# Performance work log

Measured on AMD Instinct MI355X. Metric: run time of the kernel, lower is better.

Reference implementation:

```python
import jax, jax.numpy as jnp
import numpy as np

N_NODES = 50000
N_EDGES = 800000
NODE_IN, EDGE_IN, HIDDEN, OUT = 64, 16, 128, 32


def _gcn_conv(x, edge_index, W, b, num_nodes):
    """PyG GCNConv: symmetric-normalized aggregation with self-loops.
       out = D^{-1/2} (A + I) D^{-1/2} (x @ W) + b
    """
    h = x @ W                                   # [N, H]
    loop = jnp.arange(num_nodes, dtype=edge_index.dtype)
    row = jnp.concatenate([edge_index[0], loop])  # src
    col = jnp.concatenate([edge_index[1], loop])  # dst
    deg = jax.ops.segment_sum(jnp.ones(row.shape[0], dtype=h.dtype), col,
                              num_segments=num_nodes)
    dinv = jnp.where(deg > 0, jax.lax.rsqrt(deg), 0.0)
    norm = dinv[row] * dinv[col]                # [E+N]
    msg = h[row] * norm[:, None]                # gather + scale
    out = jax.ops.segment_sum(msg, col, num_segments=num_nodes)  # scatter-add
    return out + b


def setup_inputs() -> dict:
    key = jax.random.key(0)
    ks = jax.random.split(key, 8)
    s1 = 1.0 / np.sqrt(NODE_IN)
    s2 = 1.0 / np.sqrt(HIDDEN)
    s3 = 1.0 / np.sqrt(HIDDEN * 2 + EDGE_IN)
    return {
        "x": jax.random.normal(ks[0], (N_NODES, NODE_IN), dtype=jnp.float32),
        "edge_index": jax.random.randint(ks[1], (2, N_EDGES), 0, N_NODES,
                                         dtype=jnp.int64),
        "edge_attr": jax.random.normal(ks[2], (N_EDGES, EDGE_IN),
                                       dtype=jnp.float32),
        "W1": jax.random.normal(ks[3], (NODE_IN, HIDDEN), dtype=jnp.float32) * s1,
        "b1": jnp.zeros((HIDDEN,), dtype=jnp.float32),
        "W2": jax.random.normal(ks[4], (HIDDEN, HIDDEN), dtype=jnp.float32) * s2,
        "b2": jnp.zeros((HIDDEN,), dtype=jnp.float32),
        "W_edge": jax.random.normal(ks[5], (HIDDEN * 2 + EDGE_IN, OUT),
                                    dtype=jnp.float32) * s3,
        "b_edge": jnp.zeros((OUT,), dtype=jnp.float32),
    }


def reference(x, edge_index, edge_attr, W1, b1, W2, b2, W_edge, b_edge):
    n = x.shape[0]
    h = jax.nn.relu(_gcn_conv(x, edge_index, W1, b1, n))
    h = jax.nn.relu(_gcn_conv(h, edge_index, W2, b2, n))
    src, dst = edge_index[0], edge_index[1]
    edge_features = jnp.concatenate([h[src], h[dst], edge_attr], axis=1)
    return edge_features @ W_edge + b_edge
```

## Files before the change

### kernel.cpp

```cpp
#include <hip/hip_runtime.h>

#define NN 50000
#define NE 800000

typedef __attribute__((ext_vector_type(8))) short short8v;
typedef __attribute__((ext_vector_type(4))) float f32x4;

__device__ __forceinline__ float bf_lo(unsigned u) { return __uint_as_float(u << 16); }
__device__ __forceinline__ float bf_hi(unsigned u) { return __uint_as_float(u & 0xffff0000u); }
__device__ __forceinline__ unsigned pack_bf2(float a, float b) {
  unsigned ua = __float_as_uint(a);
  ua = (ua + 0x7fffu + ((ua >> 16) & 1u)) >> 16;
  unsigned ub = __float_as_uint(b);
  ub = (ub + 0x7fffu + ((ub >> 16) & 1u)) & 0xffff0000u;
  return ua | ub;
}
__device__ __forceinline__ unsigned short bf16r(float f) {
  unsigned u = __float_as_uint(f);
  u = (u + 0x7fffu + ((u >> 16) & 1u)) >> 16;
  return (unsigned short)u;
}

__global__ void k_prep0(const float* __restrict__ W1, const float* __restrict__ W2,
                        const float* __restrict__ We,
                        unsigned short* __restrict__ W1t,
                        unsigned short* __restrict__ W2t,
                        unsigned short* __restrict__ Wabt,
                        int* cnt, int* cur) {
  int i = blockIdx.x * 256 + threadIdx.x;
  if (i < NN) { cnt[i] = 0; cur[i] = 0; }
  if (i < 8192)  { int c = i >> 6, k = i & 63;  W1t[i] = bf16r(W1[k * 128 + c]); }
  if (i < 16384) { int c = i >> 7, k = i & 127; W2t[i] = bf16r(W2[k * 128 + c]); }
  if (i < 8192) {
    int c = i >> 7, k = i & 127;
    float v = (c < 32) ? We[k * 32 + c] : We[(128 + k) * 32 + (c - 32)];
    Wabt[i] = bf16r(v);
  }
}

__global__ void k_count(const int* dst, int* cnt, int e) {
  int i = blockIdx.x * blockDim.x + threadIdx.x;
  if (i < e) atomicAdd(&cnt[dst[i]], 1);
}

__global__ void k_scan1(const int* cnt, int* offs, int* bsum, int n) {
  __shared__ int s[256];
  int i = blockIdx.x * 256 + threadIdx.x;
  int v = (i < n) ? cnt[i] : 0;
  s[threadIdx.x] = v;
  __syncthreads();
  #pragma unroll
  for (int d = 1; d < 256; d <<= 1) {
    int t = (threadIdx.x >= d) ? s[threadIdx.x - d] : 0;
    __syncthreads();
    s[threadIdx.x] += t;
    __syncthreads();
  }
  if (i < n) offs[i] = s[threadIdx.x] - v;
  if (threadIdx.x == 255) bsum[blockIdx.x] = s[255];
}

__global__ void k_scan2(int* bsum, int* offsN, int nb) {
  __shared__ int s[256];
  int v = (threadIdx.x < nb) ? bsum[threadIdx.x] : 0;
  s[threadIdx.x] = v;
  __syncthreads();
  #pragma unroll
  for (int d = 1; d < 256; d <<= 1) {
    int t = (threadIdx.x >= d) ? s[threadIdx.x - d] : 0;
    __syncthreads();
    s[threadIdx.x] += t;
    __syncthreads();
  }
  if (threadIdx.x < nb) bsum[threadIdx.x] = s[threadIdx.x] - v;
  if (threadIdx.x == 255) *offsN = s[255];
}

__global__ void k_scan3_dinv(int* offs, const int* bsum, const int* cnt,
                             float* dinv, int n) {
  int i = blockIdx.x * blockDim.x + threadIdx.x;
  if (i < n) {
    offs[i] += bsum[i >> 8];
    dinv[i] = rsqrtf((float)(cnt[i] + 1));
  }
}

__global__ void k_fill(const int* src, const int* dst, const int* offs,
                       int* cur, int* adj, int e) {
  int i = blockIdx.x * blockDim.x + threadIdx.x;
  if (i < e) {
    int d = dst[i];
    int pos = atomicAdd(&cur[d], 1);
    adj[offs[d] + pos] = src[i];
  }
}

__global__ void k_prescale(const float* __restrict__ x,
                           const float* __restrict__ dinv,
                           unsigned* __restrict__ xs, int n) {
  int i = blockIdx.x * blockDim.x + threadIdx.x;
  if (i >= n * 32) return;
  int v = i >> 5, c2 = i & 31;
  float d = dinv[v];
  float2 xv = ((const float2*)(x + (size_t)v * 64))[c2];
  xs[(size_t)v * 32 + c2] = pack_bf2(xv.x * d, xv.y * d);
}

__global__ void k_agg64(const unsigned* __restrict__ xs,
                        const int* __restrict__ offs, const int* __restrict__ adj,
                        const float* __restrict__ dinv, unsigned* __restrict__ z,
                        int n) {
  int node = blockIdx.x * 8 + (threadIdx.x >> 5);
  if (node >= n) return;
  int lane = threadIdx.x & 31;
  float ax[8], ay[8];
  {
    unsigned u = xs[(size_t)node * 32 + lane];
    ax[0] = bf_lo(u); ay[0] = bf_hi(u);
  }
  #pragma unroll
  for (int u = 1; u < 8; u++) { ax[u] = 0.f; ay[u] = 0.f; }
  int s = offs[node], e = offs[node + 1];
  int i = s;
  for (; i + 8 <= e; i += 8) {
    int idx[8];
    #pragma unroll
    for (int u = 0; u < 8; u++) idx[u] = adj[i + u];
    #pragma unroll
    for (int u = 0; u < 8; u++) {
      unsigned uv = xs[(size_t)idx[u] * 32 + lane];
      ax[u] += bf_lo(uv); ay[u] += bf_hi(uv);
    }
  }
  for (; i < e; i++) {
    unsigned uv = xs[(size_t)adj[i] * 32 + lane];
    ax[0] += bf_lo(uv); ay[0] += bf_hi(uv);
  }
  float sx = ((ax[0] + ax[1]) + (ax[2] + ax[3])) + ((ax[4] + ax[5]) + (ax[6] + ax[7]));
  float sy = ((ay[0] + ay[1]) + (ay[2] + ay[3])) + ((ay[4] + ay[5]) + (ay[6] + ay[7]));
  float d = dinv[node];
  z[(size_t)node * 32 + lane] = pack_bf2(sx * d, sy * d);
}

__global__ void k_agg128(const unsigned* __restrict__ hs,
                         const int* __restrict__ offs, const int* __restrict__ adj,
                         const float* __restrict__ dinv, unsigned* __restrict__ z,
                         int n) {
  int node = blockIdx.x * 4 + (threadIdx.x >> 6);
  if (node >= n) return;
  int lane = threadIdx.x & 63;
  float ax[8], ay[8];
  {
    unsigned u = hs[(size_t)node * 64 + lane];
    ax[0] = bf_lo(u); ay[0] = bf_hi(u);
  }
  #pragma unroll
  for (int u = 1; u < 8; u++) { ax[u] = 0.f; ay[u] = 0.f; }
  int s = offs[node], e = offs[node + 1];
  int i = s;
  for (; i + 8 <= e; i += 8) {
    int idx[8];
    #pragma unroll
    for (int u = 0; u < 8; u++) idx[u] = adj[i + u];
    #pragma unroll
    for (int u = 0; u < 8; u++) {
      unsigned uv = hs[(size_t)idx[u] * 64 + lane];
      ax[u] += bf_lo(uv); ay[u] += bf_hi(uv);
    }
  }
  for (; i < e; i++) {
    unsigned uv = hs[(size_t)adj[i] * 64 + lane];
    ax[0] += bf_lo(uv); ay[0] += bf_hi(uv);
  }
  float sx = ((ax[0] + ax[1]) + (ax[2] + ax[3])) + ((ax[4] + ax[5]) + (ax[6] + ax[7]));
  float sy = ((ay[0] + ay[1]) + (ay[2] + ay[3])) + ((ay[4] + ay[5]) + (ay[6] + ay[7]));
  float d = dinv[node];
  z[(size_t)node * 64 + lane] = pack_bf2(sx * d, sy * d);
}

template <int K>
__global__ __launch_bounds__(256) void k_mgemm(const unsigned short* __restrict__ A,
                                               const unsigned short* __restrict__ Bt,
                                               const float* __restrict__ bias,
                                               const float* __restrict__ dinv,
                                               unsigned short* __restrict__ outb,
                                               int n) {
  int lane = threadIdx.x & 63;
  int wid = threadIdx.x >> 6;
  int wr = wid >> 1, wc = wid & 1;
  int r0 = blockIdx.x * 32 + wr * 16;
  int cbase = wc * 64;
  int lr = lane & 15;
  int lk = (lane >> 4) * 8;
  int arow = r0 + lr;
  if (arow >= n) arow = n - 1;
  const unsigned short* arp = A + (size_t)arow * K + lk;
  f32x4 acc[4];
  #pragma unroll
  for (int ct = 0; ct < 4; ct++) acc[ct] = (f32x4){0.f, 0.f, 0.f, 0.f};
  #pragma unroll
  for (int ks = 0; ks < K; ks += 32) {
    short8v a = *reinterpret_cast<const short8v*>(arp + ks);
    #pragma unroll
    for (int ct = 0; ct < 4; ct++) {
      const unsigned short* bp = Bt + (size_t)(cbase + ct * 16 + lr) * K + lk + ks;
      short8v b = *reinterpret_cast<const short8v*>(bp);
      acc[ct] = __builtin_amdgcn_mfma_f32_16x16x32_bf16(a, b, acc[ct], 0, 0, 0);
    }
  }
  int rbase = r0 + (lane >> 4) * 4;
  #pragma unroll
  for (int ct = 0; ct < 4; ct++) {
    int col = cbase + ct * 16 + lr;
    float bv = bias[col];
    #pragma unroll
    for (int rg = 0; rg < 4; rg++) {
      int row = rbase + rg;
      if (row >= n) continue;
      float v = fmaxf(acc[ct][rg] + bv, 0.f);
      outb[(size_t)row * 128 + col] = bf16r(v * dinv[row]);
    }
  }
}

__global__ __launch_bounds__(256) void k_mgemm2pq(
    const unsigned short* __restrict__ A,
    const unsigned short* __restrict__ Bt,
    const unsigned short* __restrict__ Wabt,
    const float* __restrict__ bias,
    unsigned short* __restrict__ PQb,
    int n) {
  __shared__ unsigned short hs[32][136];
  int lane = threadIdx.x & 63;
  int wid = threadIdx.x >> 6;
  int wr = wid >> 1, wc = wid & 1;
  int r0 = blockIdx.x * 32;
  int lr = lane & 15;
  int lk = (lane >> 4) * 8;
  int arow = r0 + wr * 16 + lr;
  if (arow >= n) arow = n - 1;
  const unsigned short* arp = A + (size_t)arow * 128 + lk;
  f32x4 acc[4];
  #pragma unroll
  for (int ct = 0; ct < 4; ct++) acc[ct] = (f32x4){0.f, 0.f, 0.f, 0.f};
  #pragma unroll
  for (int ks = 0; ks < 128; ks += 32) {
    short8v a = *reinterpret_cast<const short8v*>(arp + ks);
    #pragma unroll
    for (int ct = 0; ct < 4; ct++) {
      const unsigned short* bp = Bt + (size_t)(wc * 64 + ct * 16 + lr) * 128 + lk + ks;
      short8v b = *reinterpret_cast<const short8v*>(bp);
      acc[ct] = __builtin_amdgcn_mfma_f32_16x16x32_bf16(a, b, acc[ct], 0, 0, 0);
    }
  }
  int rloc = wr * 16 + (lane >> 4) * 4;
  #pragma unroll
  for (int ct = 0; ct < 4; ct++) {
    int col = wc * 64 + ct * 16 + lr;
    float bv = bias[col];
    #pragma unroll
    for (int rg = 0; rg < 4; rg++)
      hs[rloc + rg][col] = bf16r(fmaxf(acc[ct][rg] + bv, 0.f));
  }
  __syncthreads();
  f32x4 acc2[2];
  acc2[0] = (f32x4){0.f, 0.f, 0.f, 0.f};
  acc2[1] = (f32x4){0.f, 0.f, 0.f, 0.f};
  #pragma unroll
  for (int ks = 0; ks < 128; ks += 32) {
    short8v a2 = *reinterpret_cast<const short8v*>(&hs[wr * 16 + lr][lk + ks]);
    #pragma unroll
    for (int ct = 0; ct < 2; ct++) {
      const unsigned short* wp = Wabt + (size_t)(wc * 32 + ct * 16 + lr) * 128 + lk + ks;
      short8v b = *reinterpret_cast<const short8v*>(wp);
      acc2[ct] = __builtin_amdgcn_mfma_f32_16x16x32_bf16(a2, b, acc2[ct], 0, 0, 0);
    }
  }
  #pragma unroll
  for (int ct = 0; ct < 2; ct++) {
    int col = wc * 32 + ct * 16 + lr;
    #pragma unroll
    for (int rg = 0; rg < 4; rg++) {
      int row = r0 + wr * 16 + (lane >> 4) * 4 + rg;
      if (row < n) PQb[(size_t)row * 64 + col] = bf16r(acc2[ct][rg]);
    }
  }
}

__global__ __launch_bounds__(256) void k_edge5(const int* __restrict__ src,
                                               const int* __restrict__ dst,
                                               const float* __restrict__ ea,
                                               const unsigned* __restrict__ PQw,
                                               const float* __restrict__ We,
                                               const float* __restrict__ be,
                                               float* __restrict__ out, int ne) {
  __shared__ int sidx[64];
  __shared__ int didx[64];
  __shared__ float eas[64][16];
  __shared__ float wcs[16][32];
  __shared__ float bes[32];
  int tid = threadIdx.x;
  int ebase = blockIdx.x * 64;
  if (tid < 128)
    ((float4*)wcs)[tid] = ((const float4*)(We + 256 * 32))[tid];
  if (tid < 32) bes[tid] = be[tid];
  if (tid >= 128 && tid < 192) sidx[tid - 128] = src[ebase + tid - 128];
  if (tid >= 192)              didx[tid - 192] = dst[ebase + tid - 192];
  {
    int row = tid >> 2, q = tid & 3;
    ((float4*)eas[row])[q] = ((const float4*)(ea + (size_t)(ebase + row) * 16))[q];
  }
  __syncthreads();
  int l = tid & 15;
  int grp = tid >> 4;
  unsigned pw[4], qw[4];
  int el[4];
  #pragma unroll
  for (int u = 0; u < 4; u++) el[u] = u * 16 + grp;
  #pragma unroll
  for (int u = 0; u < 4; u++) {
    int s = sidx[el[u]];
    int d = didx[el[u]];
    pw[u] = PQw[(size_t)s * 32 + l];
    qw[u] = PQw[(size_t)d * 32 + 16 + l];
  }
  int c0 = 2 * l;
  #pragma unroll
  for (int u = 0; u < 4; u++) {
    int e = ebase + el[u];
    float a0 = bf_lo(pw[u]) + bf_lo(qw[u]) + bes[c0];
    float a1 = bf_hi(pw[u]) + bf_hi(qw[u]) + bes[c0 + 1];
    #pragma unroll
    for (int k = 0; k < 16; k++) {
      float ev = eas[el[u]][k];
      a0 += ev * wcs[k][c0];
      a1 += ev * wcs[k][c0 + 1];
    }
    ((float2*)(out + (size_t)e * 32))[l] = make_float2(a0, a1);
  }
}

extern "C" void kernel_launch(void* const* d_in, const int* in_sizes, int n_in,
                              void* d_out, int out_size, void* d_ws, size_t ws_size,
                              hipStream_t stream) {
  const float* x  = (const float*)d_in[0];
  const int*   ei = (const int*)d_in[1];
  const float* ea = (const float*)d_in[2];
  const float* W1 = (const float*)d_in[3];
  const float* b1 = (const float*)d_in[4];
  const float* W2 = (const float*)d_in[5];
  const float* b2 = (const float*)d_in[6];
  const float* We = (const float*)d_in[7];
  const float* be = (const float*)d_in[8];
  float* out = (float*)d_out;
  const int* src = ei;
  const int* dst = ei + NE;

  char* w = (char*)d_ws;
  auto alloc = [&](size_t b) {
    void* p = (void*)w;
    w += (b + 255) & ~(size_t)255;
    return p;
  };
  int* cnt    = (int*)alloc(NN * 4);
  int* cur    = (int*)alloc(NN * 4);
  int* offs   = (int*)alloc((NN + 1) * 4);
  int* bsum   = (int*)alloc(256 * 4);
  int* adj    = (int*)alloc((size_t)NE * 4);
  float* dinv = (float*)alloc(NN * 4);
  unsigned* xs  = (unsigned*)alloc((size_t)NN * 32 * 4);
  unsigned* h1s = (unsigned*)alloc((size_t)NN * 64 * 4);
  unsigned* z12 = (unsigned*)alloc((size_t)NN * 64 * 4);
  unsigned short* w1t  = (unsigned short*)alloc(8192 * 2);
  unsigned short* w2t  = (unsigned short*)alloc(16384 * 2);
  unsigned short* wabt = (unsigned short*)alloc(8192 * 2);
  unsigned short* pqb = (unsigned short*)h1s;

  const int nblkN = (NN + 255) / 256;
  const int nblkE = (NE + 255) / 256;

  k_prep0<<<nblkN, 256, 0, stream>>>(W1, W2, We, w1t, w2t, wabt, cnt, cur);
  k_count<<<nblkE, 256, 0, stream>>>(dst, cnt, NE);
  k_scan1<<<nblkN, 256, 0, stream>>>(cnt, offs, bsum, NN);
  k_scan2<<<1, 256, 0, stream>>>(bsum, offs + NN, nblkN);
  k_scan3_dinv<<<nblkN, 256, 0, stream>>>(offs, bsum, cnt, dinv, NN);
  k_fill<<<nblkE, 256, 0, stream>>>(src, dst, offs, cur, adj, NE);

  k_prescale<<<(NN * 32 + 255) / 256, 256, 0, stream>>>(x, dinv, xs, NN);
  k_agg64<<<(NN + 7) / 8, 256, 0, stream>>>(xs, offs, adj, dinv, z12, NN);

  const int mgBlk = (NN + 31) / 32;
  k_mgemm<64><<<mgBlk, 256, 0, stream>>>((const unsigned short*)z12, w1t, b1,
                                         dinv, (unsigned short*)h1s, NN);
  k_agg128<<<(NN + 3) / 4, 256, 0, stream>>>(h1s, offs, adj, dinv, z12, NN);
  k_mgemm2pq<<<mgBlk, 256, 0, stream>>>((const unsigned short*)z12, w2t, wabt,
                                        b2, pqb, NN);
  k_edge5<<<NE / 64, 256, 0, stream>>>(src, dst, ea, (const unsigned*)pqb,
                                       We, be, out, NE);
}
```

Baseline: 243.9 us.

## Fuse neighbor aggregation into GEMM kernels and record per-edge rank during count

Each GCN layer's gather-aggregate now runs inside its MFMA GEMM kernel, staging the aggregated rows in shared memory instead of writing them to a global z buffer and reading them back. The degree-count atomics now store each edge's rank, so the CSR fill needs no second atomic pass and no cur array. Prescaling of x is merged into the scan-fixup kernel. The fused kernels process 32 nodes per block with fewer waves per node, which may reduce the memory-level parallelism available to hide gather latency.

```diff
diff --git a/kernel.cpp b/kernel.cpp
--- a/kernel.cpp
+++ b/kernel.cpp
@@ -26,9 +26,9 @@
                         unsigned short* __restrict__ W1t,
                         unsigned short* __restrict__ W2t,
                         unsigned short* __restrict__ Wabt,
-                        int* cnt, int* cur) {
+                        int* cnt) {
   int i = blockIdx.x * 256 + threadIdx.x;
-  if (i < NN) { cnt[i] = 0; cur[i] = 0; }
+  if (i < NN) cnt[i] = 0;
   if (i < 8192)  { int c = i >> 6, k = i & 63;  W1t[i] = bf16r(W1[k * 128 + c]); }
   if (i < 16384) { int c = i >> 7, k = i & 127; W2t[i] = bf16r(W2[k * 128 + c]); }
   if (i < 8192) {
@@ -38,9 +38,10 @@
   }
 }
 
-__global__ void k_count(const int* dst, int* cnt, int e) {
+__global__ void k_count(const int* __restrict__ dst, int* __restrict__ cnt,
+                        int* __restrict__ rank, int e) {
   int i = blockIdx.x * blockDim.x + threadIdx.x;
-  if (i < e) atomicAdd(&cnt[dst[i]], 1);
+  if (i < e) rank[i] = atomicAdd(&cnt[dst[i]], 1);
 }
 
 __global__ void k_scan1(const int* cnt, int* offs, int* bsum, int n) {
@@ -76,142 +77,94 @@
   if (threadIdx.x == 255) *offsN = s[255];
 }
 
-__global__ void k_scan3_dinv(int* offs, const int* bsum, const int* cnt,
-                             float* dinv, int n) {
+__global__ void k_scan3p(int* __restrict__ offs, const int* __restrict__ bsum,
+                         const int* __restrict__ cnt, float* __restrict__ dinv,
+                         const float* __restrict__ x, unsigned* __restrict__ xs) {
   int i = blockIdx.x * blockDim.x + threadIdx.x;
-  if (i < n) {
-    offs[i] += bsum[i >> 8];
-    dinv[i] = rsqrtf((float)(cnt[i] + 1));
-  }
-}
-
-__global__ void k_fill(const int* src, const int* dst, const int* offs,
-                       int* cur, int* adj, int e) {
+  if (i >= NN * 32) return;
+  int v = i >> 5, l = i & 31;
+  float d = rsqrtf((float)(cnt[v] + 1));
+  if (l == 0) {
+    offs[v] += bsum[v >> 8];
+    dinv[v] = d;
+  }
+  float2 xv = ((const float2*)(x + (size_t)v * 64))[l];
+  xs[(size_t)v * 32 + l] = pack_bf2(xv.x * d, xv.y * d);
+}
+
+__global__ void k_fill(const int* __restrict__ src, const int* __restrict__ dst,
+                       const int* __restrict__ offs, const int* __restrict__ rank,
+                       int* __restrict__ adj, int e) {
   int i = blockIdx.x * blockDim.x + threadIdx.x;
-  if (i < e) {
-    int d = dst[i];
-    int pos = atomicAdd(&cur[d], 1);
-    adj[offs[d] + pos] = src[i];
-  }
-}
-
-__global__ void k_prescale(const float* __restrict__ x,
-                           const float* __restrict__ dinv,
-                           unsigned* __restrict__ xs, int n) {
-  int i = blockIdx.x * blockDim.x + threadIdx.x;
-  if (i >= n * 32) return;
-  int v = i >> 5, c2 = i & 31;
-  float d = dinv[v];
-  float2 xv = ((const float2*)(x + (size_t)v * 64))[c2];
-  xs[(size_t)v * 32 + c2] = pack_bf2(xv.x * d, xv.y * d);
-}
-
-__global__ void k_agg64(const unsigned* __restrict__ xs,
-                        const int* __restrict__ offs, const int* __restrict__ adj,
-                        const float* __restrict__ dinv, unsigned* __restrict__ z,
-                        int n) {
-  int node = blockIdx.x * 8 + (threadIdx.x >> 5);
-  if (node >= n) return;
-  int lane = threadIdx.x & 31;
-  float ax[8], ay[8];
-  {
-    unsigned u = xs[(size_t)node * 32 + lane];
-    ax[0] = bf_lo(u); ay[0] = bf_hi(u);
-  }
-  #pragma unroll
-  for (int u = 1; u < 8; u++) { ax[u] = 0.f; ay[u] = 0.f; }
-  int s = offs[node], e = offs[node + 1];
-  int i = s;
-  for (; i + 8 <= e; i += 8) {
-    int idx[8];
-    #pragma unroll
-    for (int u = 0; u < 8; u++) idx[u] = adj[i + u];
-    #pragma unroll
-    for (int u = 0; u < 8; u++) {
-      unsigned uv = xs[(size_t)idx[u] * 32 + lane];
-      ax[u] += bf_lo(uv); ay[u] += bf_hi(uv);
-    }
-  }
-  for (; i < e; i++) {
-    unsigned uv = xs[(size_t)adj[i] * 32 + lane];
-    ax[0] += bf_lo(uv); ay[0] += bf_hi(uv);
-  }
-  float sx = ((ax[0] + ax[1]) + (ax[2] + ax[3])) + ((ax[4] + ax[5]) + (ax[6] + ax[7]));
-  float sy = ((ay[0] + ay[1]) + (ay[2] + ay[3])) + ((ay[4] + ay[5]) + (ay[6] + ay[7]));
-  float d = dinv[node];
-  z[(size_t)node * 32 + lane] = pack_bf2(sx * d, sy * d);
-}
-
-__global__ void k_agg128(const unsigned* __restrict__ hs,
-                         const int* __restrict__ offs, const int* __restrict__ adj,
-                         const float* __restrict__ dinv, unsigned* __restrict__ z,
-                         int n) {
-  int node = blockIdx.x * 4 + (threadIdx.x >> 6);
-  if (node >= n) return;
-  int lane = threadIdx.x & 63;
-  float ax[8], ay[8];
-  {
-    unsigned u = hs[(size_t)node * 64 + lane];
-    ax[0] = bf_lo(u); ay[0] = bf_hi(u);
-  }
-  #pragma unroll
-  for (int u = 1; u < 8; u++) { ax[u] = 0.f; ay[u] = 0.f; }
-  int s = offs[node], e = offs[node + 1];
-  int i = s;
-  for (; i + 8 <= e; i += 8) {
-    int idx[8];
-    #pragma unroll
-    for (int u = 0; u < 8; u++) idx[u] = adj[i + u];
-    #pragma unroll
-    for (int u = 0; u < 8; u++) {
-      unsigned uv = hs[(size_t)idx[u] * 64 + lane];
-      ax[u] += bf_lo(uv); ay[u] += bf_hi(uv);
-    }
-  }
-  for (; i < e; i++) {
-    unsigned uv = hs[(size_t)adj[i] * 64 + lane];
-    ax[0] += bf_lo(uv); ay[0] += bf_hi(uv);
-  }
-  float sx = ((ax[0] + ax[1]) + (ax[2] + ax[3])) + ((ax[4] + ax[5]) + (ax[6] + ax[7]));
-  float sy = ((ay[0] + ay[1]) + (ay[2] + ay[3])) + ((ay[4] + ay[5]) + (ay[6] + ay[7]));
-  float d = dinv[node];
-  z[(size_t)node * 64 + lane] = pack_bf2(sx * d, sy * d);
-}
-
-template <int K>
-__global__ __launch_bounds__(256) void k_mgemm(const unsigned short* __restrict__ A,
-                                               const unsigned short* __restrict__ Bt,
-                                               const float* __restrict__ bias,
-                                               const float* __restrict__ dinv,
-                                               unsigned short* __restrict__ outb,
-                                               int n) {
+  if (i < e) adj[offs[dst[i]] + rank[i]] = src[i];
+}
+
+__global__ __launch_bounds__(256) void k_aggemm1(
+    const unsigned* __restrict__ xs, const int* __restrict__ offs,
+    const int* __restrict__ adj, const float* __restrict__ dinv,
+    const unsigned short* __restrict__ Bt,
+    const float* __restrict__ bias,
+    unsigned short* __restrict__ outb,
+    int n) {
+  __shared__ unsigned zd[32][36];
   int lane = threadIdx.x & 63;
   int wid = threadIdx.x >> 6;
+  int r0 = blockIdx.x * 32;
+  int h = lane >> 5, hl = lane & 31;
+  for (int it = 0; it < 4; it++) {
+    int loc = wid * 8 + it * 2 + h;
+    int node = r0 + loc;
+    if (node >= n) node = n - 1;
+    float ax[8], ay[8];
+    {
+      unsigned u = xs[(size_t)node * 32 + hl];
+      ax[0] = bf_lo(u); ay[0] = bf_hi(u);
+    }
+    #pragma unroll
+    for (int u = 1; u < 8; u++) { ax[u] = 0.f; ay[u] = 0.f; }
+    int s = offs[node], e = offs[node + 1];
+    int i = s;
+    for (; i + 8 <= e; i += 8) {
+      int idx[8];
+      #pragma unroll
+      for (int u = 0; u < 8; u++) idx[u] = adj[i + u];
+      #pragma unroll
+      for (int u = 0; u < 8; u++) {
+        unsigned uv = xs[(size_t)idx[u] * 32 + hl];
+        ax[u] += bf_lo(uv); ay[u] += bf_hi(uv);
+      }
+    }
+    for (; i < e; i++) {
+      unsigned uv = xs[(size_t)adj[i] * 32 + hl];
+      ax[0] += bf_lo(uv); ay[0] += bf_hi(uv);
+    }
+    float sx = ((ax[0] + ax[1]) + (ax[2] + ax[3])) + ((ax[4] + ax[5]) + (ax[6] + ax[7]));
+    float sy = ((ay[0] + ay[1]) + (ay[2] + ay[3])) + ((ay[4] + ay[5]) + (ay[6] + ay[7]));
+    float d = dinv[node];
+    zd[loc][hl] = pack_bf2(sx * d, sy * d);
+  }
+  __syncthreads();
   int wr = wid >> 1, wc = wid & 1;
-  int r0 = blockIdx.x * 32 + wr * 16;
-  int cbase = wc * 64;
   int lr = lane & 15;
   int lk = (lane >> 4) * 8;
-  int arow = r0 + lr;
-  if (arow >= n) arow = n - 1;
-  const unsigned short* arp = A + (size_t)arow * K + lk;
   f32x4 acc[4];
   #pragma unroll
   for (int ct = 0; ct < 4; ct++) acc[ct] = (f32x4){0.f, 0.f, 0.f, 0.f};
   #pragma unroll
-  for (int ks = 0; ks < K; ks += 32) {
-    short8v a = *reinterpret_cast<const short8v*>(arp + ks);
+  for (int ks = 0; ks < 64; ks += 32) {
+    short8v a = *reinterpret_cast<const short8v*>(
+        (const unsigned short*)&zd[wr * 16 + lr][0] + lk + ks);
     #pragma unroll
     for (int ct = 0; ct < 4; ct++) {
-      const unsigned short* bp = Bt + (size_t)(cbase + ct * 16 + lr) * K + lk + ks;
+      const unsigned short* bp = Bt + (size_t)(wc * 64 + ct * 16 + lr) * 64 + lk + ks;
       short8v b = *reinterpret_cast<const short8v*>(bp);
       acc[ct] = __builtin_amdgcn_mfma_f32_16x16x32_bf16(a, b, acc[ct], 0, 0, 0);
     }
   }
-  int rbase = r0 + (lane >> 4) * 4;
+  int rbase = r0 + wr * 16 + (lane >> 4) * 4;
   #pragma unroll
   for (int ct = 0; ct < 4; ct++) {
-    int col = cbase + ct * 16 + lr;
+    int col = wc * 64 + ct * 16 + lr;
     float bv = bias[col];
     #pragma unroll
     for (int rg = 0; rg < 4; rg++) {
@@ -223,29 +176,63 @@
   }
 }
 
-__global__ __launch_bounds__(256) void k_mgemm2pq(
-    const unsigned short* __restrict__ A,
+__global__ __launch_bounds__(256) void k_aggemm2(
+    const unsigned* __restrict__ hw,
+    const int* __restrict__ offs, const int* __restrict__ adj,
+    const float* __restrict__ dinv,
     const unsigned short* __restrict__ Bt,
     const unsigned short* __restrict__ Wabt,
     const float* __restrict__ bias,
     unsigned short* __restrict__ PQb,
     int n) {
-  __shared__ unsigned short hs[32][136];
+  __shared__ unsigned ztd[32][68];
+  __shared__ unsigned short hs2[32][136];
   int lane = threadIdx.x & 63;
   int wid = threadIdx.x >> 6;
+  int r0 = blockIdx.x * 32;
+  for (int it = 0; it < 8; it++) {
+    int loc = wid * 8 + it;
+    int node = r0 + loc;
+    if (node >= n) node = n - 1;
+    float ax[8], ay[8];
+    {
+      unsigned u = hw[(size_t)node * 64 + lane];
+      ax[0] = bf_lo(u); ay[0] = bf_hi(u);
+    }
+    #pragma unroll
+    for (int u = 1; u < 8; u++) { ax[u] = 0.f; ay[u] = 0.f; }
+    int s = offs[node], e = offs[node + 1];
+    int i = s;
+    for (; i + 8 <= e; i += 8) {
+      int idx[8];
+      #pragma unroll
+      for (int u = 0; u < 8; u++) idx[u] = adj[i + u];
+      #pragma unroll
+      for (int u = 0; u < 8; u++) {
+        unsigned uv = hw[(size_t)idx[u] * 64 + lane];
+        ax[u] += bf_lo(uv); ay[u] += bf_hi(uv);
+      }
+    }
+    for (; i < e; i++) {
+      unsigned uv = hw[(size_t)adj[i] * 64 + lane];
+      ax[0] += bf_lo(uv); ay[0] += bf_hi(uv);
+    }
+    float sx = ((ax[0] + ax[1]) + (ax[2] + ax[3])) + ((ax[4] + ax[5]) + (ax[6] + ax[7]));
+    float sy = ((ay[0] + ay[1]) + (ay[2] + ay[3])) + ((ay[4] + ay[5]) + (ay[6] + ay[7]));
+    float d = dinv[node];
+    ztd[loc][lane] = pack_bf2(sx * d, sy * d);
+  }
+  __syncthreads();
   int wr = wid >> 1, wc = wid & 1;
-  int r0 = blockIdx.x * 32;
   int lr = lane & 15;
   int lk = (lane >> 4) * 8;
-  int arow = r0 + wr * 16 + lr;
-  if (arow >= n) arow = n - 1;
-  const unsigned short* arp = A + (size_t)arow * 128 + lk;
   f32x4 acc[4];
   #pragma unroll
   for (int ct = 0; ct < 4; ct++) acc[ct] = (f32x4){0.f, 0.f, 0.f, 0.f};
   #pragma unroll
   for (int ks = 0; ks < 128; ks += 32) {
-    short8v a = *reinterpret_cast<const short8v*>(arp + ks);
+    short8v a = *reinterpret_cast<const short8v*>(
+        (const unsigned short*)&ztd[wr * 16 + lr][0] + lk + ks);
     #pragma unroll
     for (int ct = 0; ct < 4; ct++) {
       const unsigned short* bp = Bt + (size_t)(wc * 64 + ct * 16 + lr) * 128 + lk + ks;
@@ -260,7 +247,7 @@
     float bv = bias[col];
     #pragma unroll
     for (int rg = 0; rg < 4; rg++)
-      hs[rloc + rg][col] = bf16r(fmaxf(acc[ct][rg] + bv, 0.f));
+      hs2[rloc + rg][col] = bf16r(fmaxf(acc[ct][rg] + bv, 0.f));
   }
   __syncthreads();
   f32x4 acc2[2];
@@ -268,7 +255,7 @@
   acc2[1] = (f32x4){0.f, 0.f, 0.f, 0.f};
   #pragma unroll
   for (int ks = 0; ks < 128; ks += 32) {
-    short8v a2 = *reinterpret_cast<const short8v*>(&hs[wr * 16 + lr][lk + ks]);
+    short8v a2 = *reinterpret_cast<const short8v*>(&hs2[wr * 16 + lr][lk + ks]);
     #pragma unroll
     for (int ct = 0; ct < 2; ct++) {
       const unsigned short* wp = Wabt + (size_t)(wc * 32 + ct * 16 + lr) * 128 + lk + ks;
@@ -363,38 +350,33 @@
     return p;
   };
   int* cnt    = (int*)alloc(NN * 4);
-  int* cur    = (int*)alloc(NN * 4);
   int* offs   = (int*)alloc((NN + 1) * 4);
   int* bsum   = (int*)alloc(256 * 4);
   int* adj    = (int*)alloc((size_t)NE * 4);
+  int* rank   = (int*)alloc((size_t)NE * 4);
   float* dinv = (float*)alloc(NN * 4);
   unsigned* xs  = (unsigned*)alloc((size_t)NN * 32 * 4);
   unsigned* h1s = (unsigned*)alloc((size_t)NN * 64 * 4);
-  unsigned* z12 = (unsigned*)alloc((size_t)NN * 64 * 4);
+  unsigned short* pqb  = (unsigned short*)alloc((size_t)NN * 64 * 2);
   unsigned short* w1t  = (unsigned short*)alloc(8192 * 2);
   unsigned short* w2t  = (unsigned short*)alloc(16384 * 2);
   unsigned short* wabt = (unsigned short*)alloc(8192 * 2);
-  unsigned short* pqb = (unsigned short*)h1s;
 
   const int nblkN = (NN + 255) / 256;
   const int nblkE = (NE + 255) / 256;
 
-  k_prep0<<<nblkN, 256, 0, stream>>>(W1, W2, We, w1t, w2t, wabt, cnt, cur);
-  k_count<<<nblkE, 256, 0, stream>>>(dst, cnt, NE);
+  k_prep0<<<nblkN, 256, 0, stream>>>(W1, W2, We, w1t, w2t, wabt, cnt);
+  k_count<<<nblkE, 256, 0, stream>>>(dst, cnt, rank, NE);
   k_scan1<<<nblkN, 256, 0, stream>>>(cnt, offs, bsum, NN);
   k_scan2<<<1, 256, 0, stream>>>(bsum, offs + NN, nblkN);
-  k_scan3_dinv<<<nblkN, 256, 0, stream>>>(offs, bsum, cnt, dinv, NN);
-  k_fill<<<nblkE, 256, 0, stream>>>(src, dst, offs, cur, adj, NE);
-
-  k_prescale<<<(NN * 32 + 255) / 256, 256, 0, stream>>>(x, dinv, xs, NN);
-  k_agg64<<<(NN + 7) / 8, 256, 0, stream>>>(xs, offs, adj, dinv, z12, NN);
+  k_scan3p<<<(NN * 32 + 255) / 256, 256, 0, stream>>>(offs, bsum, cnt, dinv, x, xs);
+  k_fill<<<nblkE, 256, 0, stream>>>(src, dst, offs, rank, adj, NE);
 
   const int mgBlk = (NN + 31) / 32;
-  k_mgemm<64><<<mgBlk, 256, 0, stream>>>((const unsigned short*)z12, w1t, b1,
-                                         dinv, (unsigned short*)h1s, NN);
-  k_agg128<<<(NN + 3) / 4, 256, 0, stream>>>(h1s, offs, adj, dinv, z12, NN);
-  k_mgemm2pq<<<mgBlk, 256, 0, stream>>>((const unsigned short*)z12, w2t, wabt,
-                                        b2, pqb, NN);
+  k_aggemm1<<<mgBlk, 256, 0, stream>>>(xs, offs, adj, dinv, w1t, b1,
+                                       (unsigned short*)h1s, NN);
+  k_aggemm2<<<mgBlk, 256, 0, stream>>>(h1s, offs, adj, dinv, w2t, wabt, b2,
+                                       pqb, NN);
   k_edge5<<<NE / 64, 256, 0, stream>>>(src, dst, ea, (const unsigned*)pqb,
                                        We, be, out, NE);
 }
```

Result: no change. 239.9 us (-1.6%).
